# Optimization experiments

Hardware: AMD Instinct MI355X
Metric: run time of the kernel (lower is better)

Reference implementation:

```python
import jax, jax.numpy as jnp
import numpy as np

N_WORDS = 30000
EMB_DIM = 784
MAT_DIM = 28  # sqrt(784)
BATCH = 1024
SEQ = 64


def setup_inputs() -> dict:
    key = jax.random.key(0)
    k_sent, k_w = jax.random.split(key)
    sent = jax.random.randint(k_sent, (BATCH, SEQ), 0, N_WORDS + 1, dtype=jnp.int64 if jax.config.jax_enable_x64 else jnp.int32)
    # cmow 'identity' init: N(0, 0.1) + flattened identity; row 0 is the neutral element (identity matrix)
    eye_flat = jnp.eye(MAT_DIM, dtype=jnp.float32).reshape(1, EMB_DIM)
    init_w = 0.1 * jax.random.normal(k_w, (N_WORDS, EMB_DIM), dtype=jnp.float32) + eye_flat
    table = jnp.concatenate([eye_flat, init_w], axis=0)  # [N_WORDS+1, 784]
    return {"sent": sent, "table": table}


def reference(sent, table):
    B, S = sent.shape
    # embedding lookup, view as per-word matrices: [B, S, 28, 28]
    mats = table[sent].reshape(B, S, MAT_DIM, MAT_DIM)
    # left-to-right matrix chain product: cur = cur @ mats[:, i]
    def step(carry, m):
        return jnp.matmul(carry, m), None
    # seq-major for scan: [S-1, B, 28, 28]
    rest = jnp.swapaxes(mats[:, 1:], 0, 1)
    prod, _ = jax.lax.scan(step, mats[:, 0], rest)
    return prod.reshape(B, EMB_DIM)  # flatten matrix -> [B, 784]
```

## Files before the change

### kernel.cpp

```cpp
#include <hip/hip_runtime.h>
#include <hip/hip_bf16.h>


#define MD    28
#define MD2   784
#define SEQL  64
#define CHUNK 8
#define WPB   8

typedef __attribute__((ext_vector_type(8))) short bf16x8;
typedef __attribute__((ext_vector_type(4))) float floatx4;

#define LDS_FENCE() asm volatile("s_waitcnt lgkmcnt(0)" ::: "memory")

__device__ __forceinline__ unsigned short f2bf(float x) {
    unsigned u = __float_as_uint(x);
    unsigned r = u + 0x7FFFu + ((u >> 16) & 1u);
    return (unsigned short)(r >> 16);
}
__device__ __forceinline__ float bf2f(unsigned short h) {
    return __uint_as_float(((unsigned)h) << 16);
}

__device__ __forceinline__ unsigned pk_bf16(float x, float y) {
    float2 f; f.x = x; f.y = y;
    __hip_bfloat162 h2 = __float22bfloat162_rn(f);
    union { __hip_bfloat162 h; unsigned u; } cv; cv.h = h2;
    return cv.u;
}

union U4F { uint4 u; bf16x8 v; };

__device__ __forceinline__ void pack8m(const float* v, unsigned m01, unsigned m23,
                                       bf16x8* hi, bf16x8* lo) {
    U4F H, L;
    unsigned* ph = (unsigned*)&H.u;
    unsigned* pl = (unsigned*)&L.u;
    #pragma unroll
    for (int p = 0; p < 4; ++p) {
        float x = v[2*p], y = v[2*p+1];
        unsigned h = pk_bf16(x, y);
        float rx = x - __uint_as_float(h << 16);
        float ry = y - __uint_as_float(h & 0xffff0000u);
        pl[p] = pk_bf16(rx, ry);
        ph[p] = h;
    }
    H.u.x &= m01; H.u.y &= m01; H.u.z &= m23; H.u.w &= m23;
    L.u.x &= m01; L.u.y &= m01; L.u.z &= m23; L.u.w &= m23;
    *hi = H.v; *lo = L.v;
}

__device__ __forceinline__ void pack8(const float* v, bf16x8* hi, bf16x8* lo) {
    pack8m(v, ~0u, ~0u, hi, lo);
}

__device__ __forceinline__ int xaddr(int n, int g, int h) {
    return n * 64 + ((h ^ (n & 1)) << 5) + ((g ^ ((n >> 1) & 3)) << 3);
}

struct Acc { floatx4 t[2][2]; };

__device__ __forceinline__ void acc_zero(Acc& a) {
    #pragma unroll
    for (int mi = 0; mi < 2; ++mi)
        #pragma unroll
        for (int ni = 0; ni < 2; ++ni)
            a.t[mi][ni] = (floatx4){0.f, 0.f, 0.f, 0.f};
}

__device__ __forceinline__ floatx4 mfma16(bf16x8 a, bf16x8 b, floatx4 c) {
    return __builtin_amdgcn_mfma_f32_16x16x32_bf16(a, b, c, 0, 0, 0);
}

__device__ __forceinline__ void mm12(bf16x8 ah0, bf16x8 ah1, bf16x8 al0, bf16x8 al1,
                                     bf16x8 bh0, bf16x8 bh1, bf16x8 bl0, bf16x8 bl1,
                                     Acc& acc) {
    acc.t[0][0] = mfma16(ah0, bh0, acc.t[0][0]);
    acc.t[0][1] = mfma16(ah0, bh1, acc.t[0][1]);
    acc.t[1][0] = mfma16(ah1, bh0, acc.t[1][0]);
    acc.t[1][1] = mfma16(ah1, bh1, acc.t[1][1]);
    acc.t[0][0] = mfma16(ah0, bl0, acc.t[0][0]);
    acc.t[0][1] = mfma16(ah0, bl1, acc.t[0][1]);
    acc.t[1][0] = mfma16(ah1, bl0, acc.t[1][0]);
    acc.t[1][1] = mfma16(ah1, bl1, acc.t[1][1]);
    acc.t[0][0] = mfma16(al0, bh0, acc.t[0][0]);
    acc.t[0][1] = mfma16(al0, bh1, acc.t[0][1]);
    acc.t[1][0] = mfma16(al1, bh0, acc.t[1][0]);
    acc.t[1][1] = mfma16(al1, bh1, acc.t[1][1]);
}

__device__ __forceinline__ void readB(const unsigned short* X, int n16, int q,
                                      bf16x8* bh0, bf16x8* bh1, bf16x8* bl0, bf16x8* bl1) {
    *bh0 = *(const bf16x8*)(X + xaddr(n16,      q, 0));
    *bl0 = *(const bf16x8*)(X + xaddr(n16,      q, 1));
    *bh1 = *(const bf16x8*)(X + xaddr(16 + n16, q, 0));
    *bl1 = *(const bf16x8*)(X + xaddr(16 + n16, q, 1));
}

__device__ __forceinline__ void writeX(unsigned short* X, const Acc& acc,
                                       int n16, int q) {
    const int sub = (q & 1) * 4;
    #pragma unroll
    for (int mi = 0; mi < 2; ++mi) {
        const int g = 2 * mi + (q >> 1);
        #pragma unroll
        for (int ni = 0; ni < 2; ++ni) {
            floatx4 a = acc.t[mi][ni];
            const int n = ni * 16 + n16;
            unsigned h0 = pk_bf16(a[0], a[1]);
            unsigned h1 = pk_bf16(a[2], a[3]);
            float r0 = a[0] - __uint_as_float(h0 << 16);
            float r1 = a[1] - __uint_as_float(h0 & 0xffff0000u);
            float r2 = a[2] - __uint_as_float(h1 << 16);
            float r3 = a[3] - __uint_as_float(h1 & 0xffff0000u);
            unsigned l0 = pk_bf16(r0, r1);
            unsigned l1 = pk_bf16(r2, r3);
            uint2 uh; uh.x = h0; uh.y = h1;
            uint2 ul; ul.x = l0; ul.y = l1;
            *(uint2*)(X + xaddr(n, g, 0) + sub) = uh;
            *(uint2*)(X + xaddr(n, g, 1) + sub) = ul;
        }
    }
}

__device__ __forceinline__ void writeAconv(unsigned short* P, const Acc& acc,
                                           int n16, int q) {
    unsigned short* Sh = P;
    unsigned short* Sl = P + 1024;
    #pragma unroll
    for (int mi = 0; mi < 2; ++mi)
        #pragma unroll
        for (int ni = 0; ni < 2; ++ni) {
            floatx4 a = acc.t[mi][ni];
            #pragma unroll
            for (int r = 0; r < 4; ++r) {
                int m = mi * 16 + q * 4 + r;
                int n = ni * 16 + n16;
                int off = m * 32 + n;
                unsigned short hh = f2bf(a[r]);
                Sh[off] = hh;
                Sl[off] = f2bf(a[r] - bf2f(hh));
            }
        }
}

__device__ __forceinline__ void readAconv(const unsigned short* P, int n16, int q,
                                          bf16x8* ah0, bf16x8* ah1,
                                          bf16x8* al0, bf16x8* al1) {
    const unsigned short* Sh = P;
    const unsigned short* Sl = P + 1024;
    const int o0 = n16 * 32 + 8 * q;
    const int o1 = (16 + n16) * 32 + 8 * q;
    *ah0 = *(const bf16x8*)(Sh + o0);
    *ah1 = *(const bf16x8*)(Sh + o1);
    *al0 = *(const bf16x8*)(Sl + o0);
    *al1 = *(const bf16x8*)(Sl + o1);
}

__global__ __launch_bounds__(512, 4)
void cmow_mfma_kernel(const int* __restrict__ sent,
                      const float* __restrict__ table,
                      float* __restrict__ out)
{
    __shared__ __align__(16) unsigned short smem[WPB * 2048];

    const int tid  = threadIdx.x;
    const int lane = tid & 63;
    const int w    = tid >> 6;
    const int b    = blockIdx.x;

    unsigned short* Xw = smem + w * 2048;

    const int* sp = sent + b * SEQL + w * CHUNK;
    int idx[CHUNK];
    #pragma unroll
    for (int i = 0; i < CHUNK; ++i) idx[i] = sp[i];

    const int n16 = lane & 15;
    const int q   = lane >> 4;

    const int colB  = (n16 < 12) ? (16 + n16) : 0;
    const int offA0 = (8 * q) * MD + n16;
    const int offA4 = ((q == 3) ? 0 : (8 * q + 4) * MD) + n16;
    const int offB0 = (8 * q) * MD + colB;
    const int offB4 = ((q == 3) ? 0 : (8 * q + 4) * MD) + colB;
    const unsigned mA23 = (q == 3) ? 0u : ~0u;
    const unsigned mB01 = (n16 < 12) ? ~0u : 0u;
    const unsigned mB23 = (n16 < 12 && q != 3) ? ~0u : 0u;

    {
        const int nr = lane & 31;
        const int h2 = lane >> 5;
        float v[16];
        #pragma unroll
        for (int t = 0; t < 16; ++t) v[t] = 0.f;
        if (nr < MD) {
            const float* src = table + (size_t)idx[0] * MD2 + nr * MD + 16 * h2;
            const int nval = (h2 == 0) ? 16 : 12;
            #pragma unroll
            for (int t = 0; t < 16; t += 4) {
                if (t < nval) {
                    float4 f = *(const float4*)(src + t);
                    v[t] = f.x; v[t+1] = f.y; v[t+2] = f.z; v[t+3] = f.w;
                }
            }
        }
        #pragma unroll
        for (int s = 0; s < 2; ++s) {
            bf16x8 hi, lo;
            pack8(v + 8 * s, &hi, &lo);
            int g = 2 * h2 + s;
            *(bf16x8*)(Xw + xaddr(nr, g, 0)) = hi;
            *(bf16x8*)(Xw + xaddr(nr, g, 1)) = lo;
        }
    }

    float pa[8], pb[8];
    {
        const float* bp = table + (size_t)idx[1] * MD2;
        #pragma unroll
        for (int j = 0; j < 4; ++j) {
            pa[j]     = bp[offA0 + j * MD];
            pb[j]     = bp[offB0 + j * MD];
            pa[4 + j] = bp[offA4 + j * MD];
            pb[4 + j] = bp[offB4 + j * MD];
        }
    }

    for (int i = 1; i < CHUNK; ++i) {
        bf16x8 ah0, ah1, al0, al1;
        pack8m(pa, ~0u,  mA23, &ah0, &al0);
        pack8m(pb, mB01, mB23, &ah1, &al1);

        if (i + 1 < CHUNK) {
            const float* bp = table + (size_t)idx[i + 1] * MD2;
            #pragma unroll
            for (int j = 0; j < 4; ++j) {
                pa[j]     = bp[offA0 + j * MD];
                pb[j]     = bp[offB0 + j * MD];
                pa[4 + j] = bp[offA4 + j * MD];
                pb[4 + j] = bp[offB4 + j * MD];
            }
        }

        LDS_FENCE();

        bf16x8 bh0, bh1, bl0, bl1;
        readB(Xw, n16, q, &bh0, &bh1, &bl0, &bl1);

        Acc acc; acc_zero(acc);
        mm12(ah0, ah1, al0, al1, bh0, bh1, bl0, bl1, acc);

        if (i < CHUNK - 1 || (w & 1) == 0)
            writeX(Xw, acc, n16, q);
        else
            writeAconv(Xw, acc, n16, q);
    }

    __syncthreads();

    if (w < 4) {
        bf16x8 ah0, ah1, al0, al1, bh0, bh1, bl0, bl1;
        readAconv(smem + (2 * w + 1) * 2048, n16, q, &ah0, &ah1, &al0, &al1);
        readB(smem + (2 * w) * 2048, n16, q, &bh0, &bh1, &bl0, &bl1);
        Acc acc; acc_zero(acc);
        mm12(ah0, ah1, al0, al1, bh0, bh1, bl0, bl1, acc);
        if ((w & 1) == 0) writeX(smem + (2 * w) * 2048, acc, n16, q);
        else              writeAconv(smem + (2 * w + 1) * 2048, acc, n16, q);
    }
    __syncthreads();

    if (w < 2) {
        bf16x8 ah0, ah1, al0, al1, bh0, bh1, bl0, bl1;
        readAconv(smem + (4 * w + 3) * 2048, n16, q, &ah0, &ah1, &al0, &al1);
        readB(smem + (4 * w) * 2048, n16, q, &bh0, &bh1, &bl0, &bl1);
        Acc acc; acc_zero(acc);
        mm12(ah0, ah1, al0, al1, bh0, bh1, bl0, bl1, acc);
        if (w == 0) writeX(smem, acc, n16, q);
        else        writeAconv(smem + 7 * 2048, acc, n16, q);
    }
    __syncthreads();

    if (w == 0) {
        bf16x8 ah0, ah1, al0, al1, bh0, bh1, bl0, bl1;
        readAconv(smem + 7 * 2048, n16, q, &ah0, &ah1, &al0, &al1);
        readB(smem, n16, q, &bh0, &bh1, &bl0, &bl1);
        Acc acc; acc_zero(acc);
        mm12(ah0, ah1, al0, al1, bh0, bh1, bl0, bl1, acc);

        float* op = out + (size_t)b * MD2;
        #pragma unroll
        for (int mi = 0; mi < 2; ++mi)
            #pragma unroll
            for (int ni = 0; ni < 2; ++ni) {
                int C = ni * 16 + n16;
                int R = mi * 16 + q * 4;
                if (C < MD && R + 3 < MD) {
                    floatx4 a = acc.t[mi][ni];
                    float4 st; st.x = a[0]; st.y = a[1]; st.z = a[2]; st.w = a[3];
                    *(float4*)(op + C * MD + R) = st;
                }
            }
    }
}

extern "C" void kernel_launch(void* const* d_in, const int* in_sizes, int n_in,
                              void* d_out, int out_size, void* d_ws, size_t ws_size,
                              hipStream_t stream) {
    const int*   sent  = (const int*)d_in[0];
    const float* table = (const float*)d_in[1];
    float*       outp  = (float*)d_out;

    const int batch = in_sizes[0] / SEQL;
    cmow_mfma_kernel<<<dim3(batch), dim3(512), 0, stream>>>(sent, table, outp);
}
```

Measured before the change: 152.7 us.

## Split sequence across 16 waves of 4 words with generalized tree reduction

Each block now runs 16 waves of 4 sequence elements each instead of 8 waves of 8, which halves the serial matrix-multiply chain per wave. The hand-written three-level reduction becomes a generic log-depth loop with one extra level. The prefetch of the second matrix is moved ahead of the first matrix's conversion so global loads overlap better. The cost is more reduction levels and barriers, twice the LDS per block, and possibly lower occupancy with 1024-thread blocks.

Result: slower. 165.2 us (+8.2%).

```diff
diff --git a/kernel.cpp b/kernel.cpp
--- a/kernel.cpp
+++ b/kernel.cpp
@@ -5,8 +5,8 @@
 #define MD    28
 #define MD2   784
 #define SEQL  64
-#define CHUNK 8
-#define WPB   8
+#define CHUNK 4
+#define WPB   16
 
 typedef __attribute__((ext_vector_type(8))) short bf16x8;
 typedef __attribute__((ext_vector_type(4))) float floatx4;
@@ -157,7 +157,7 @@
     *al1 = *(const bf16x8*)(Sl + o1);
 }
 
-__global__ __launch_bounds__(512, 4)
+__global__ __launch_bounds__(1024, 4)
 void cmow_mfma_kernel(const int* __restrict__ sent,
                       const float* __restrict__ table,
                       float* __restrict__ out)
@@ -187,6 +187,18 @@
     const unsigned mA23 = (q == 3) ? 0u : ~0u;
     const unsigned mB01 = (n16 < 12) ? ~0u : 0u;
     const unsigned mB23 = (n16 < 12 && q != 3) ? ~0u : 0u;
+
+    float pa[8], pb[8];
+    {
+        const float* bp = table + (size_t)idx[1] * MD2;
+        #pragma unroll
+        for (int j = 0; j < 4; ++j) {
+            pa[j]     = bp[offA0 + j * MD];
+            pb[j]     = bp[offB0 + j * MD];
+            pa[4 + j] = bp[offA4 + j * MD];
+            pb[4 + j] = bp[offB4 + j * MD];
+        }
+    }
 
     {
         const int nr = lane & 31;
@@ -215,18 +227,6 @@
         }
     }
 
-    float pa[8], pb[8];
-    {
-        const float* bp = table + (size_t)idx[1] * MD2;
-        #pragma unroll
-        for (int j = 0; j < 4; ++j) {
-            pa[j]     = bp[offA0 + j * MD];
-            pb[j]     = bp[offB0 + j * MD];
-            pa[4 + j] = bp[offA4 + j * MD];
-            pb[4 + j] = bp[offB4 + j * MD];
-        }
-    }
-
     for (int i = 1; i < CHUNK; ++i) {
         bf16x8 ah0, ah1, al0, al1;
         pack8m(pa, ~0u,  mA23, &ah0, &al0);
@@ -257,50 +257,40 @@
             writeAconv(Xw, acc, n16, q);
     }
 
-    __syncthreads();
-
-    if (w < 4) {
-        bf16x8 ah0, ah1, al0, al1, bh0, bh1, bl0, bl1;
-        readAconv(smem + (2 * w + 1) * 2048, n16, q, &ah0, &ah1, &al0, &al1);
-        readB(smem + (2 * w) * 2048, n16, q, &bh0, &bh1, &bl0, &bl1);
-        Acc acc; acc_zero(acc);
-        mm12(ah0, ah1, al0, al1, bh0, bh1, bl0, bl1, acc);
-        if ((w & 1) == 0) writeX(smem + (2 * w) * 2048, acc, n16, q);
-        else              writeAconv(smem + (2 * w + 1) * 2048, acc, n16, q);
-    }
-    __syncthreads();
-
-    if (w < 2) {
-        bf16x8 ah0, ah1, al0, al1, bh0, bh1, bl0, bl1;
-        readAconv(smem + (4 * w + 3) * 2048, n16, q, &ah0, &ah1, &al0, &al1);
-        readB(smem + (4 * w) * 2048, n16, q, &bh0, &bh1, &bl0, &bl1);
-        Acc acc; acc_zero(acc);
-        mm12(ah0, ah1, al0, al1, bh0, bh1, bl0, bl1, acc);
-        if (w == 0) writeX(smem, acc, n16, q);
-        else        writeAconv(smem + 7 * 2048, acc, n16, q);
-    }
-    __syncthreads();
-
-    if (w == 0) {
-        bf16x8 ah0, ah1, al0, al1, bh0, bh1, bl0, bl1;
-        readAconv(smem + 7 * 2048, n16, q, &ah0, &ah1, &al0, &al1);
-        readB(smem, n16, q, &bh0, &bh1, &bl0, &bl1);
-        Acc acc; acc_zero(acc);
-        mm12(ah0, ah1, al0, al1, bh0, bh1, bl0, bl1, acc);
-
-        float* op = out + (size_t)b * MD2;
-        #pragma unroll
-        for (int mi = 0; mi < 2; ++mi)
-            #pragma unroll
-            for (int ni = 0; ni < 2; ++ni) {
-                int C = ni * 16 + n16;
-                int R = mi * 16 + q * 4;
-                if (C < MD && R + 3 < MD) {
-                    floatx4 a = acc.t[mi][ni];
-                    float4 st; st.x = a[0]; st.y = a[1]; st.z = a[2]; st.w = a[3];
-                    *(float4*)(op + C * MD + R) = st;
-                }
+    float* op = out + (size_t)b * MD2;
+
+    #pragma unroll
+    for (int S = 1; S <= WPB / 2; S <<= 1) {
+        const int act = WPB / (2 * S);
+        __syncthreads();
+        if (w < act) {
+            const int pA = (2 * w + 1) * S + S - 1;
+            const int pB = 2 * w * S;
+            bf16x8 ah0, ah1, al0, al1, bh0, bh1, bl0, bl1;
+            readAconv(smem + pA * 2048, n16, q, &ah0, &ah1, &al0, &al1);
+            readB(smem + pB * 2048, n16, q, &bh0, &bh1, &bl0, &bl1);
+            Acc acc; acc_zero(acc);
+            mm12(ah0, ah1, al0, al1, bh0, bh1, bl0, bl1, acc);
+
+            if (act == 1) {
+                #pragma unroll
+                for (int mi = 0; mi < 2; ++mi)
+                    #pragma unroll
+                    for (int ni = 0; ni < 2; ++ni) {
+                        int C = ni * 16 + n16;
+                        int R = mi * 16 + q * 4;
+                        if (C < MD && R + 3 < MD) {
+                            floatx4 a = acc.t[mi][ni];
+                            float4 st; st.x = a[0]; st.y = a[1]; st.z = a[2]; st.w = a[3];
+                            *(float4*)(op + C * MD + R) = st;
+                        }
+                    }
+            } else if ((w & 1) == 0) {
+                writeX(smem + pB * 2048, acc, n16, q);
+            } else {
+                writeAconv(smem + pA * 2048, acc, n16, q);
             }
+        }
     }
 }
 
@@ -312,5 +302,5 @@
     float*       outp  = (float*)d_out;
 
     const int batch = in_sizes[0] / SEQL;
-    cmow_mfma_kernel<<<dim3(batch), dim3(512), 0, stream>>>(sent, table, outp);
-}
+    cmow_mfma_kernel<<<dim3(batch), dim3(1024), 0, stream>>>(sent, table, outp);
+}
```
